# Kernel tuning notes

Hardware: AMD Instinct MI355X
Metric: run time of the kernel (lower is better)

Reference implementation:

```python
import jax, jax.numpy as jnp
import numpy as np

B, H, L, C = 16, 512, 4096, 1
LAM = 0.001  # kernel squash threshold (lam in LongConvKernel)


def setup_inputs() -> dict:
    key = jax.random.key(0)
    ks = jax.random.split(key, 5)
    u = jax.random.normal(ks[0], (B, H, L), jnp.float32)
    # LongConvKernel 'double_exp' init: K ~ N(0, 0.02^2) * exp(-(j/L) * (H//2)^(i/H))
    K = jax.random.normal(ks[1], (C, H, L), jnp.float32) * 0.02
    i = jnp.arange(H, dtype=jnp.float32)[:, None]
    j = jnp.arange(L, dtype=jnp.float32)[None, :]
    double_exp = jnp.exp(-(j / L) * jnp.power(float(H // 2), i / H))  # (H, L)
    kernel = K * double_exp[None]
    D = jax.random.normal(ks[2], (C, H), jnp.float32)  # skip connection params
    # TransposedLinear(C*H -> H): weight (d_output, d_input), kaiming-ish scale
    Wout = jax.random.normal(ks[3], (H, C * H), jnp.float32) / np.sqrt(C * H)
    bout = jax.random.normal(ks[4], (H,), jnp.float32) * 0.01
    return {"u": u, "kernel": kernel, "D": D, "Wout": Wout, "bout": bout}


def reference(u, kernel, D, Wout, bout):
    Lseq = u.shape[-1]
    # kernel squashing: relu(|k| - lam) * sign(k)  (soft-threshold)
    k = jax.nn.relu(jnp.abs(kernel) - LAM) * jnp.sign(kernel)  # (C, H, L)
    n = 2 * Lseq
    k_f = jnp.fft.rfft(k, n=n, axis=-1)            # (C, H, n//2+1) complex
    u_f = jnp.fft.rfft(u, n=n, axis=-1)            # (B, H, n//2+1) complex
    y_f = jnp.einsum('bhl,chl->bchl', u_f, k_f)    # pointwise multiply in freq
    y = jnp.fft.irfft(y_f, n=n, axis=-1)[..., :Lseq]  # (B, C, H, L)
    y = y + jnp.einsum('bhl,ch->bchl', u, D)       # skip term
    y = y.reshape(y.shape[0], C * H, Lseq)         # (B, C*H, L)
    y = jax.nn.gelu(y, approximate=False)          # activation (torch GELU = exact)
    # output_linear: TransposedLinear + swish postact
    y = jnp.einsum('bul,vu->bvl', y, Wout) + bout[None, :, None]
    y = jax.nn.silu(y)
    return y
```

## Files before the change

kernel.cpp:

```cpp
#include <hip/hip_runtime.h>
#include <hip/hip_bf16.h>
#include <math.h>

#define BB 16
#define HH 512
#define LL 4096
#define NFFT 8192
#define LAM 0.001f

typedef __attribute__((ext_vector_type(8))) short short8;
typedef __attribute__((ext_vector_type(4))) float floatx4;

__device__ __forceinline__ void cmul(float ar, float ai, float br, float bi,
                                     float& cr, float& ci) {
  cr = ar * br - ai * bi;
  ci = ar * bi + ai * br;
}

constexpr float W16C[10] = {1.f, 0.92387953f, 0.70710678f, 0.38268343f, 0.f,
                            -0.38268343f, -0.70710678f, -0.92387953f, -1.f, -0.92387953f};
constexpr float W16S[10] = {0.f, -0.38268343f, -0.70710678f, -0.92387953f, -1.f,
                            -0.92387953f, -0.70710678f, -0.38268343f, 0.f, 0.38268343f};
constexpr float W32C[16] = {1.f, 0.98078528f, 0.92387953f, 0.83146961f, 0.70710678f,
                            0.55557023f, 0.38268343f, 0.19509032f, 0.f, -0.19509032f,
                            -0.38268343f, -0.55557023f, -0.70710678f, -0.83146961f,
                            -0.92387953f, -0.98078528f};
constexpr float W32S[16] = {0.f, -0.19509032f, -0.38268343f, -0.55557023f, -0.70710678f,
                            -0.83146961f, -0.92387953f, -0.98078528f, -1.f, -0.98078528f,
                            -0.92387953f, -0.83146961f, -0.70710678f, -0.55557023f,
                            -0.38268343f, -0.19509032f};

__device__ __forceinline__ void fft16_f(float* xr, float* xi) {
  float yr[16], yi[16];
#pragma unroll
  for (int j = 0; j < 4; ++j) {
    float t0r = xr[j] + xr[j + 8],      t0i = xi[j] + xi[j + 8];
    float t1r = xr[j] - xr[j + 8],      t1i = xi[j] - xi[j + 8];
    float t2r = xr[j + 4] + xr[j + 12], t2i = xi[j + 4] + xi[j + 12];
    float t3r = xr[j + 4] - xr[j + 12], t3i = xi[j + 4] - xi[j + 12];
    float o0r = t0r + t2r, o0i = t0i + t2i;
    float o1r = t1r + t3i, o1i = t1i - t3r;
    float o2r = t0r - t2r, o2i = t0i - t2i;
    float o3r = t1r - t3i, o3i = t1i + t3r;
    yr[j] = o0r; yi[j] = o0i;
    if (j == 0) {
      yr[4] = o1r; yi[4] = o1i; yr[8] = o2r; yi[8] = o2i; yr[12] = o3r; yi[12] = o3i;
    } else {
      cmul(o1r, o1i, W16C[j], W16S[j], yr[j + 4], yi[j + 4]);
      cmul(o2r, o2i, W16C[2 * j], W16S[2 * j], yr[j + 8], yi[j + 8]);
      cmul(o3r, o3i, W16C[3 * j], W16S[3 * j], yr[j + 12], yi[j + 12]);
    }
  }
#pragma unroll
  for (int m = 0; m < 4; ++m) {
    float t0r = yr[4 * m] + yr[4 * m + 2],     t0i = yi[4 * m] + yi[4 * m + 2];
    float t1r = yr[4 * m] - yr[4 * m + 2],     t1i = yi[4 * m] - yi[4 * m + 2];
    float t2r = yr[4 * m + 1] + yr[4 * m + 3], t2i = yi[4 * m + 1] + yi[4 * m + 3];
    float t3r = yr[4 * m + 1] - yr[4 * m + 3], t3i = yi[4 * m + 1] - yi[4 * m + 3];
    xr[m] = t0r + t2r;       xi[m] = t0i + t2i;
    xr[m + 4] = t1r + t3i;   xi[m + 4] = t1i - t3r;
    xr[m + 8] = t0r - t2r;   xi[m + 8] = t0i - t2i;
    xr[m + 12] = t1r - t3i;  xi[m + 12] = t1i + t3r;
  }
}

__device__ __forceinline__ void ifft16_f(float* xr, float* xi) {
  float yr[16], yi[16];
#pragma unroll
  for (int m = 0; m < 4; ++m) {
    float t0r = xr[m] + xr[m + 8],      t0i = xi[m] + xi[m + 8];
    float t1r = xr[m] - xr[m + 8],      t1i = xi[m] - xi[m + 8];
    float t2r = xr[m + 4] + xr[m + 12], t2i = xi[m + 4] + xi[m + 12];
    float t3r = xr[m + 4] - xr[m + 12], t3i = xi[m + 4] - xi[m + 12];
    yr[4 * m] = t0r + t2r;     yi[4 * m] = t0i + t2i;
    yr[4 * m + 1] = t1r - t3i; yi[4 * m + 1] = t1i + t3r;
    yr[4 * m + 2] = t0r - t2r; yi[4 * m + 2] = t0i - t2i;
    yr[4 * m + 3] = t1r + t3i; yi[4 * m + 3] = t1i - t3r;
  }
#pragma unroll
  for (int j = 0; j < 4; ++j) {
    float v0r = yr[j], v0i = yi[j];
    float v1r, v1i, v2r, v2i, v3r, v3i;
    if (j == 0) {
      v1r = yr[4]; v1i = yi[4]; v2r = yr[8]; v2i = yi[8]; v3r = yr[12]; v3i = yi[12];
    } else {
      cmul(yr[j + 4], yi[j + 4], W16C[j], -W16S[j], v1r, v1i);
      cmul(yr[j + 8], yi[j + 8], W16C[2 * j], -W16S[2 * j], v2r, v2i);
      cmul(yr[j + 12], yi[j + 12], W16C[3 * j], -W16S[3 * j], v3r, v3i);
    }
    float t0r = v0r + v2r, t0i = v0i + v2i;
    float t1r = v0r - v2r, t1i = v0i - v2i;
    float t2r = v1r + v3r, t2i = v1i + v3i;
    float t3r = v1r - v3r, t3i = v1i - v3i;
    xr[j] = t0r + t2r;       xi[j] = t0i + t2i;
    xr[j + 4] = t1r - t3i;   xi[j + 4] = t1i + t3r;
    xr[j + 8] = t0r - t2r;   xi[j + 8] = t0i - t2i;
    xr[j + 12] = t1r + t3i;  xi[j + 12] = t1i - t3r;
  }
}

__device__ __forceinline__ float gelu_exact(float y) {
  return 0.5f * y * (1.f + erff(y * 0.70710678118654752f));
}

__global__ __launch_bounds__(512) void twgen_kernel(float4* __restrict__ tw1,
                                                    float4* __restrict__ tw2) {
  const int j = threadIdx.x;
  const int m2 = blockIdx.x;
  float s0, c0, s1, c1;
  const float a1 = -6.283185307179586f / 8192.f;
  sincosf(a1 * (float)(j * (2 * m2)), &s0, &c0);
  sincosf(a1 * (float)(j * (2 * m2 + 1)), &s1, &c1);
  tw1[m2 * 512 + j] = make_float4(c0, s0, c1, s1);
  if (j < 32) {
    const float a2 = -6.283185307179586f / 512.f;
    sincosf(a2 * (float)(j * (2 * m2)), &s0, &c0);
    sincosf(a2 * (float)(j * (2 * m2 + 1)), &s1, &c1);
    tw2[m2 * 32 + j] = make_float4(c0, s0, c1, s1);
  }
}

__global__ void wconv_kernel(const float* __restrict__ W,
                             __hip_bfloat16* __restrict__ Wb) {
  int i = blockIdx.x * 256 + threadIdx.x;
  Wb[i] = __float2bfloat16(W[i]);
}

__global__ __launch_bounds__(512)
void kf_kernel(const float* __restrict__ kern, const float* __restrict__ D,
               float* __restrict__ Kf, const float4* __restrict__ tw1,
               const float4* __restrict__ tw2) {
  __shared__ __align__(16) float sre[NFFT];
  __shared__ __align__(16) float sim[NFFT];
  const int t = threadIdx.x;
  const int h = blockIdx.x;
  const float* kr = kern + (size_t)h * LL;

  {
    const int j = t;
    float xr[16], xi[16];
#pragma unroll
    for (int r = 0; r < 8; ++r) {
      float kv = kr[j + 512 * r];
      float a = fabsf(kv) - LAM;
      float sq = (a > 0.f) ? ((kv > 0.f) ? a : -a) : 0.f;
      xr[r] = sq * (1.0f / (float)NFFT);
      xi[r] = 0.f;
    }
#pragma unroll
    for (int r = 8; r < 16; ++r) { xr[r] = 0.f; xi[r] = 0.f; }
    fft16_f(xr, xi);
    const int jx = j ^ (((j >> 5) & 7) << 2);
#pragma unroll
    for (int m2 = 0; m2 < 8; ++m2) {
      float4 w = tw1[m2 * 512 + j];
      float tr, ti;
      cmul(xr[2 * m2], xi[2 * m2], w.x, w.y, tr, ti);
      sre[jx + 512 * (2 * m2)] = tr; sim[jx + 512 * (2 * m2)] = ti;
      cmul(xr[2 * m2 + 1], xi[2 * m2 + 1], w.z, w.w, tr, ti);
      sre[jx + 512 * (2 * m2 + 1)] = tr; sim[jx + 512 * (2 * m2 + 1)] = ti;
    }
  }
  __syncthreads();

  {
    const int jj = t & 31, gg = t >> 5;
    const int base = gg * 512 + jj;
    float xr[16], xi[16];
#pragma unroll
    for (int m = 0; m < 16; ++m) {
      const int a = (base + 32 * m) ^ ((m & 7) << 2);
      xr[m] = sre[a]; xi[m] = sim[a];
    }
    fft16_f(xr, xi);
#pragma unroll
    for (int m2 = 0; m2 < 8; ++m2) {
      float4 w = tw2[m2 * 32 + jj];
      float tr, ti;
      int a0 = (base + 32 * (2 * m2)) ^ (((2 * m2) & 7) << 2);
      cmul(xr[2 * m2], xi[2 * m2], w.x, w.y, tr, ti);
      sre[a0] = tr; sim[a0] = ti;
      int a1 = (base + 32 * (2 * m2 + 1)) ^ (((2 * m2 + 1) & 7) << 2);
      cmul(xr[2 * m2 + 1], xi[2 * m2 + 1], w.z, w.w, tr, ti);
      sre[a1] = tr; sim[a1] = ti;
    }
  }
  __syncthreads();

  {
    const int k = t >> 1, par = t & 1;
    const int kx = k & 7;
    const float sgn = par ? -1.f : 1.f;
    float xr[16], xi[16];
#pragma unroll
    for (int c = 0; c < 4; ++c) {
      float4 lr = ((const float4*)sre)[8 * k + (c ^ kx)];
      float4 hr = ((const float4*)sre)[8 * k + ((c + 4) ^ kx)];
      float4 li = ((const float4*)sim)[8 * k + (c ^ kx)];
      float4 hi4 = ((const float4*)sim)[8 * k + ((c + 4) ^ kx)];
      float vr[4] = {lr.x + sgn * hr.x, lr.y + sgn * hr.y, lr.z + sgn * hr.z, lr.w + sgn * hr.w};
      float vi[4] = {li.x + sgn * hi4.x, li.y + sgn * hi4.y, li.z + sgn * hi4.z, li.w + sgn * hi4.w};
#pragma unroll
      for (int e = 0; e < 4; ++e) {
        const int j = 4 * c + e;
        const float twr = par ? W32C[j] : 1.f;
        const float tws = par ? W32S[j] : 0.f;
        cmul(vr[e], vi[e], twr, tws, xr[j], xi[j]);
      }
    }
    fft16_f(xr, xi);
    const float dsc = D[h] * (1.0f / (float)NFFT);
    float4* out4 = (float4*)(Kf + (size_t)h * NFFT * 2) + 8 * t;
#pragma unroll
    for (int c = 0; c < 8; ++c)
      out4[c] = make_float4(xr[2 * c] + dsc, xi[2 * c], xr[2 * c + 1] + dsc, xi[2 * c + 1]);
  }
}

__global__ __launch_bounds__(512)
void fftconv_kernel(
    const float* __restrict__ u, const float* __restrict__ Kf,
    __hip_bfloat16* __restrict__ g, const float4* __restrict__ tw1,
    const float4* __restrict__ tw2) {
  __shared__ __align__(16) float sre[NFFT];
  __shared__ __align__(16) float sim[NFFT];
  const int t = threadIdx.x;
  const int h = blockIdx.x;
  const int p = blockIdx.y;
  const int b0 = 2 * p, b1 = 2 * p + 1;
  const float* u0 = u + ((size_t)(b0 * HH + h)) * LL;
  const float* u1 = u + ((size_t)(b1 * HH + h)) * LL;

  const int jx = t ^ (((t >> 5) & 7) << 2);

  {
    const int j = t;
    float xr[16], xi[16];
#pragma unroll
    for (int r = 0; r < 8; ++r) {
      xr[r] = u0[j + 512 * r];
      xi[r] = u1[j + 512 * r];
    }
#pragma unroll
    for (int r = 8; r < 16; ++r) { xr[r] = 0.f; xi[r] = 0.f; }
    fft16_f(xr, xi);
#pragma unroll
    for (int m2 = 0; m2 < 8; ++m2) {
      float4 w = tw1[m2 * 512 + j];
      float tr, ti;
      cmul(xr[2 * m2], xi[2 * m2], w.x, w.y, tr, ti);
      sre[jx + 512 * (2 * m2)] = tr; sim[jx + 512 * (2 * m2)] = ti;
      cmul(xr[2 * m2 + 1], xi[2 * m2 + 1], w.z, w.w, tr, ti);
      sre[jx + 512 * (2 * m2 + 1)] = tr; sim[jx + 512 * (2 * m2 + 1)] = ti;
    }
  }
  __syncthreads();

  {
    const int jj = t & 31, gg = t >> 5;
    const int base = gg * 512 + jj;
    float xr[16], xi[16];
#pragma unroll
    for (int m = 0; m < 16; ++m) {
      const int a = (base + 32 * m) ^ ((m & 7) << 2);
      xr[m] = sre[a]; xi[m] = sim[a];
    }
    fft16_f(xr, xi);
#pragma unroll
    for (int m2 = 0; m2 < 8; ++m2) {
      float4 w = tw2[m2 * 32 + jj];
      float tr, ti;
      int a0 = (base + 32 * (2 * m2)) ^ (((2 * m2) & 7) << 2);
      cmul(xr[2 * m2], xi[2 * m2], w.x, w.y, tr, ti);
      sre[a0] = tr; sim[a0] = ti;
      int a1 = (base + 32 * (2 * m2 + 1)) ^ (((2 * m2 + 1) & 7) << 2);
      cmul(xr[2 * m2 + 1], xi[2 * m2 + 1], w.z, w.w, tr, ti);
      sre[a1] = tr; sim[a1] = ti;
    }
  }
  __syncthreads();

  {
    const int k = t >> 1, par = t & 1;
    const int kx = k & 7;
    const float sgn = par ? -1.f : 1.f;
    float xr[16], xi[16];
#pragma unroll
    for (int c = 0; c < 4; ++c) {
      float4 lr = ((const float4*)sre)[8 * k + (c ^ kx)];
      float4 hr = ((const float4*)sre)[8 * k + ((c + 4) ^ kx)];
      float4 li = ((const float4*)sim)[8 * k + (c ^ kx)];
      float4 hi4 = ((const float4*)sim)[8 * k + ((c + 4) ^ kx)];
      float vr[4] = {lr.x + sgn * hr.x, lr.y + sgn * hr.y, lr.z + sgn * hr.z, lr.w + sgn * hr.w};
      float vi[4] = {li.x + sgn * hi4.x, li.y + sgn * hi4.y, li.z + sgn * hi4.z, li.w + sgn * hi4.w};
#pragma unroll
      for (int e = 0; e < 4; ++e) {
        const int j = 4 * c + e;
        const float twr = par ? W32C[j] : 1.f;
        const float tws = par ? W32S[j] : 0.f;
        cmul(vr[e], vi[e], twr, tws, xr[j], xi[j]);
      }
    }
    fft16_f(xr, xi);
    const float4* kf4 = (const float4*)(Kf + (size_t)h * NFFT * 2) + 8 * t;
#pragma unroll
    for (int c = 0; c < 8; ++c) {
      float4 kk = kf4[c];
      float tr, ti;
      cmul(xr[2 * c], xi[2 * c], kk.x, kk.y, tr, ti);
      xr[2 * c] = tr; xi[2 * c] = ti;
      cmul(xr[2 * c + 1], xi[2 * c + 1], kk.z, kk.w, tr, ti);
      xr[2 * c + 1] = tr; xi[2 * c + 1] = ti;
    }
    ifft16_f(xr, xi);
    float outr[16], outi[16];
#pragma unroll
    for (int j = 0; j < 16; ++j) {
      float pr, pi;
      if (par) cmul(xr[j], xi[j], W32C[j], -W32S[j], pr, pi);
      else { pr = xr[j]; pi = xi[j]; }
      float qr = __shfl_xor(pr, 1);
      float qi = __shfl_xor(pi, 1);
      outr[j] = par ? (qr - pr) : (pr + qr);
      outi[j] = par ? (qi - pi) : (pi + qi);
    }
#pragma unroll
    for (int c = 0; c < 4; ++c) {
      const int q = (4 * par + c) ^ kx;
      ((float4*)sre)[8 * k + q] = make_float4(outr[4 * c], outr[4 * c + 1], outr[4 * c + 2], outr[4 * c + 3]);
      ((float4*)sim)[8 * k + q] = make_float4(outi[4 * c], outi[4 * c + 1], outi[4 * c + 2], outi[4 * c + 3]);
    }
  }
  __syncthreads();

  {
    const int jj = t & 31, gg = t >> 5;
    const int base = gg * 512 + jj;
    float yr[16], yi[16];
#pragma unroll
    for (int m2 = 0; m2 < 8; ++m2) {
      float4 w = tw2[m2 * 32 + jj];
      int a0 = (base + 32 * (2 * m2)) ^ (((2 * m2) & 7) << 2);
      cmul(sre[a0], sim[a0], w.x, -w.y, yr[2 * m2], yi[2 * m2]);
      int a1 = (base + 32 * (2 * m2 + 1)) ^ (((2 * m2 + 1) & 7) << 2);
      cmul(sre[a1], sim[a1], w.z, -w.w, yr[2 * m2 + 1], yi[2 * m2 + 1]);
    }
    ifft16_f(yr, yi);
#pragma unroll
    for (int m = 0; m < 16; ++m) {
      const int a = (base + 32 * m) ^ ((m & 7) << 2);
      sre[a] = yr[m]; sim[a] = yi[m];
    }
  }
  __syncthreads();

  {
    const int j = t;
    float yr[16], yi[16];
#pragma unroll
    for (int m2 = 0; m2 < 8; ++m2) {
      float4 w = tw1[m2 * 512 + j];
      cmul(sre[jx + 512 * (2 * m2)], sim[jx + 512 * (2 * m2)], w.x, -w.y,
           yr[2 * m2], yi[2 * m2]);
      cmul(sre[jx + 512 * (2 * m2 + 1)], sim[jx + 512 * (2 * m2 + 1)], w.z, -w.w,
           yr[2 * m2 + 1], yi[2 * m2 + 1]);
    }
    ifft16_f(yr, yi);
    __hip_bfloat16* g0 = g + ((size_t)(b0 * HH + h)) * LL;
    __hip_bfloat16* g1 = g + ((size_t)(b1 * HH + h)) * LL;
#pragma unroll
    for (int r = 0; r < 8; ++r) {
      g0[j + 512 * r] = __float2bfloat16(gelu_exact(yr[r]));
      g1[j + 512 * r] = __float2bfloat16(gelu_exact(yi[r]));
    }
  }
}

__global__ __launch_bounds__(256) void transpose_kernel(
    const __hip_bfloat16* __restrict__ g, __hip_bfloat16* __restrict__ g2) {
  __shared__ unsigned short tile[64][72];
  const int lb = blockIdx.x;
  const int hb = blockIdx.y;
  const int b = blockIdx.z;
  const int l0 = lb * 64, h0 = hb * 64;
  const int tid = threadIdx.x;
  const int r = tid >> 3;
  const int gc = tid & 7;
  const int c = gc * 8;
  const unsigned short* gs = (const unsigned short*)g;
  unsigned short* g2s = (unsigned short*)g2;
  for (int it = 0; it < 2; ++it) {
    int rr = r + it * 32;
    int4 v = *(const int4*)(gs + ((size_t)(b * HH + h0 + rr)) * LL + l0 + c);
    *(int4*)&tile[rr][(gc ^ (rr >> 3)) << 3] = v;
  }
  __syncthreads();
  for (int it = 0; it < 2; ++it) {
    int rr = r + it * 32;
    const int pc = (rr & 7) | (((rr >> 3) ^ gc) << 3);
    unsigned short vals[8];
#pragma unroll
    for (int j = 0; j < 8; ++j) vals[j] = tile[c + j][pc];
    *(int4*)(g2s + ((size_t)(b * LL + l0 + rr)) * HH + h0 + c) = *(int4*)vals;
  }
}

__global__ __launch_bounds__(256, 4) void gemm_kernel(
    const __hip_bfloat16* __restrict__ Wb, const __hip_bfloat16* __restrict__ g2,
    const float* __restrict__ bout, float* __restrict__ out) {
  const int vt = blockIdx.x;
  const int lt = blockIdx.y;
  const int b = blockIdx.z;
  const int wave = threadIdx.x >> 6;
  const int ln = threadIdx.x & 63;
  const int wr = wave >> 1, wc = wave & 1;
  const int vbase = vt * 128 + wr * 64;
  const int lbase = lt * 128 + wc * 64;
  const int lane16 = ln & 15;
  const int quad = ln >> 4;

  floatx4 acc[4][4];
#pragma unroll
  for (int mi = 0; mi < 4; ++mi)
#pragma unroll
    for (int ni = 0; ni < 4; ++ni) acc[mi][ni] = (floatx4){0.f, 0.f, 0.f, 0.f};

  const unsigned short* A = (const unsigned short*)Wb;
  const unsigned short* Bm = (const unsigned short*)g2 + (size_t)b * LL * HH;

  for (int k0 = 0; k0 < HH; k0 += 32) {
    const int kk = k0 + quad * 8;
    short8 af[4], bf[4];
#pragma unroll
    for (int mi = 0; mi < 4; ++mi) {
      const int m = vbase + mi * 16 + lane16;
      af[mi] = *(const short8*)(A + (size_t)m * HH + kk);
    }
#pragma unroll
    for (int ni = 0; ni < 4; ++ni) {
      const int n = lbase + ni * 16 + lane16;
      bf[ni] = *(const short8*)(Bm + (size_t)n * HH + kk);
    }
#pragma unroll
    for (int mi = 0; mi < 4; ++mi)
#pragma unroll
      for (int ni = 0; ni < 4; ++ni)
        acc[mi][ni] = __builtin_amdgcn_mfma_f32_16x16x32_bf16(af[mi], bf[ni],
                                                              acc[mi][ni], 0, 0, 0);
  }

#pragma unroll
  for (int mi = 0; mi < 4; ++mi) {
#pragma unroll
    for (int r = 0; r < 4; ++r) {
      const int m = vbase + mi * 16 + quad * 4 + r;
      const float bias = bout[m];
#pragma unroll
      for (int ni = 0; ni < 4; ++ni) {
        const int n = lbase + ni * 16 + lane16;
        float y = acc[mi][ni][r] + bias;
        y = y / (1.f + __expf(-y));
        out[((size_t)(b * HH + m)) * LL + n] = y;
      }
    }
  }
}

extern "C" void kernel_launch(void* const* d_in, const int* in_sizes, int n_in,
                              void* d_out, int out_size, void* d_ws, size_t ws_size,
                              hipStream_t stream) {
  const float* u = (const float*)d_in[0];
  const float* kern = (const float*)d_in[1];
  const float* D = (const float*)d_in[2];
  const float* Wout = (const float*)d_in[3];
  const float* bout = (const float*)d_in[4];
  float* out = (float*)d_out;

  char* ws = (char*)d_ws;
  const size_t KF_BYTES = (size_t)HH * NFFT * sizeof(float2);
  const size_t G_BYTES = (size_t)BB * HH * LL * 2;
  float* Kf = (float*)ws;
  __hip_bfloat16* g = (__hip_bfloat16*)(ws + KF_BYTES);
  __hip_bfloat16* g2 = (__hip_bfloat16*)(ws + KF_BYTES + G_BYTES);
  __hip_bfloat16* Wb = (__hip_bfloat16*)(ws + KF_BYTES + 2 * G_BYTES);
  float4* tw1 = (float4*)g2;
  float4* tw2 = tw1 + 8 * 512;

  twgen_kernel<<<dim3(8), dim3(512), 0, stream>>>(tw1, tw2);
  wconv_kernel<<<dim3((HH * HH) / 256), dim3(256), 0, stream>>>(Wout, Wb);
  kf_kernel<<<dim3(HH), dim3(512), 0, stream>>>(kern, D, Kf, tw1, tw2);
  fftconv_kernel<<<dim3(HH, BB / 2), dim3(512), 0, stream>>>(u, Kf, g, tw1, tw2);
  transpose_kernel<<<dim3(LL / 64, HH / 64, BB), dim3(256), 0, stream>>>(g, g2);
  gemm_kernel<<<dim3(HH / 128, LL / 128, BB), dim3(256), 0, stream>>>(Wb, g2, bout, out);
}
```

Measured before the change: 588.8 us.

## Restructure 8192-point FFT as radix-8 passes with 1024 threads and interleaved smem

Replaces the radix-16/32 three-pass FFT (512 threads, 16 complex values per thread, split re/im shared arrays) with a radix-8 decomposition: 1024 threads each hold 8 values across four passes. Shared memory becomes one interleaved float2 array with an XOR swizzle, and twiddle tables are regenerated in bit-reversed order. The goal is lower register pressure and more threads per block, better latency hiding and fewer bank conflicts. In exchange it adds extra synchronised passes through shared memory and more block-level barriers.

```diff
diff --git a/kernel.cpp b/kernel.cpp
--- a/kernel.cpp
+++ b/kernel.cpp
@@ -11,112 +11,200 @@
 typedef __attribute__((ext_vector_type(8))) short short8;
 typedef __attribute__((ext_vector_type(4))) float floatx4;
 
+#define R2C 0.70710678118654752f
+
 __device__ __forceinline__ void cmul(float ar, float ai, float br, float bi,
                                      float& cr, float& ci) {
   cr = ar * br - ai * bi;
   ci = ar * bi + ai * br;
 }
 
-constexpr float W16C[10] = {1.f, 0.92387953f, 0.70710678f, 0.38268343f, 0.f,
-                            -0.38268343f, -0.70710678f, -0.92387953f, -1.f, -0.92387953f};
-constexpr float W16S[10] = {0.f, -0.38268343f, -0.70710678f, -0.92387953f, -1.f,
-                            -0.92387953f, -0.70710678f, -0.38268343f, 0.f, 0.38268343f};
-constexpr float W32C[16] = {1.f, 0.98078528f, 0.92387953f, 0.83146961f, 0.70710678f,
-                            0.55557023f, 0.38268343f, 0.19509032f, 0.f, -0.19509032f,
-                            -0.38268343f, -0.55557023f, -0.70710678f, -0.83146961f,
-                            -0.92387953f, -0.98078528f};
-constexpr float W32S[16] = {0.f, -0.19509032f, -0.38268343f, -0.55557023f, -0.70710678f,
-                            -0.83146961f, -0.92387953f, -0.98078528f, -1.f, -0.98078528f,
-                            -0.92387953f, -0.83146961f, -0.70710678f, -0.55557023f,
-                            -0.38268343f, -0.19509032f};
-
-__device__ __forceinline__ void fft16_f(float* xr, float* xi) {
-  float yr[16], yi[16];
-#pragma unroll
-  for (int j = 0; j < 4; ++j) {
-    float t0r = xr[j] + xr[j + 8],      t0i = xi[j] + xi[j + 8];
-    float t1r = xr[j] - xr[j + 8],      t1i = xi[j] - xi[j + 8];
-    float t2r = xr[j + 4] + xr[j + 12], t2i = xi[j + 4] + xi[j + 12];
-    float t3r = xr[j + 4] - xr[j + 12], t3i = xi[j + 4] - xi[j + 12];
-    float o0r = t0r + t2r, o0i = t0i + t2i;
-    float o1r = t1r + t3i, o1i = t1i - t3r;
-    float o2r = t0r - t2r, o2i = t0i - t2i;
-    float o3r = t1r - t3i, o3i = t1i + t3r;
-    yr[j] = o0r; yi[j] = o0i;
-    if (j == 0) {
-      yr[4] = o1r; yi[4] = o1i; yr[8] = o2r; yi[8] = o2i; yr[12] = o3r; yi[12] = o3i;
-    } else {
-      cmul(o1r, o1i, W16C[j], W16S[j], yr[j + 4], yi[j + 4]);
-      cmul(o2r, o2i, W16C[2 * j], W16S[2 * j], yr[j + 8], yi[j + 8]);
-      cmul(o3r, o3i, W16C[3 * j], W16S[3 * j], yr[j + 12], yi[j + 12]);
-    }
-  }
-#pragma unroll
-  for (int m = 0; m < 4; ++m) {
-    float t0r = yr[4 * m] + yr[4 * m + 2],     t0i = yi[4 * m] + yi[4 * m + 2];
-    float t1r = yr[4 * m] - yr[4 * m + 2],     t1i = yi[4 * m] - yi[4 * m + 2];
-    float t2r = yr[4 * m + 1] + yr[4 * m + 3], t2i = yi[4 * m + 1] + yi[4 * m + 3];
-    float t3r = yr[4 * m + 1] - yr[4 * m + 3], t3i = yi[4 * m + 1] - yi[4 * m + 3];
-    xr[m] = t0r + t2r;       xi[m] = t0i + t2i;
-    xr[m + 4] = t1r + t3i;   xi[m + 4] = t1i - t3r;
-    xr[m + 8] = t0r - t2r;   xi[m + 8] = t0i - t2i;
-    xr[m + 12] = t1r - t3i;  xi[m + 12] = t1i + t3r;
-  }
-}
-
-__device__ __forceinline__ void ifft16_f(float* xr, float* xi) {
-  float yr[16], yi[16];
-#pragma unroll
-  for (int m = 0; m < 4; ++m) {
-    float t0r = xr[m] + xr[m + 8],      t0i = xi[m] + xi[m + 8];
-    float t1r = xr[m] - xr[m + 8],      t1i = xi[m] - xi[m + 8];
-    float t2r = xr[m + 4] + xr[m + 12], t2i = xi[m + 4] + xi[m + 12];
-    float t3r = xr[m + 4] - xr[m + 12], t3i = xi[m + 4] - xi[m + 12];
-    yr[4 * m] = t0r + t2r;     yi[4 * m] = t0i + t2i;
-    yr[4 * m + 1] = t1r - t3i; yi[4 * m + 1] = t1i + t3r;
-    yr[4 * m + 2] = t0r - t2r; yi[4 * m + 2] = t0i - t2i;
-    yr[4 * m + 3] = t1r + t3i; yi[4 * m + 3] = t1i - t3r;
-  }
-#pragma unroll
-  for (int j = 0; j < 4; ++j) {
-    float v0r = yr[j], v0i = yi[j];
-    float v1r, v1i, v2r, v2i, v3r, v3i;
-    if (j == 0) {
-      v1r = yr[4]; v1i = yi[4]; v2r = yr[8]; v2i = yi[8]; v3r = yr[12]; v3i = yi[12];
-    } else {
-      cmul(yr[j + 4], yi[j + 4], W16C[j], -W16S[j], v1r, v1i);
-      cmul(yr[j + 8], yi[j + 8], W16C[2 * j], -W16S[2 * j], v2r, v2i);
-      cmul(yr[j + 12], yi[j + 12], W16C[3 * j], -W16S[3 * j], v3r, v3i);
-    }
-    float t0r = v0r + v2r, t0i = v0i + v2i;
-    float t1r = v0r - v2r, t1i = v0i - v2i;
-    float t2r = v1r + v3r, t2i = v1i + v3i;
-    float t3r = v1r - v3r, t3i = v1i - v3i;
-    xr[j] = t0r + t2r;       xi[j] = t0i + t2i;
-    xr[j + 4] = t1r - t3i;   xi[j + 4] = t1i + t3r;
-    xr[j + 8] = t0r - t2r;   xi[j + 8] = t0i - t2i;
-    xr[j + 12] = t1r + t3i;  xi[j + 12] = t1i - t3r;
-  }
+constexpr float W16C[8] = {1.f, 0.92387953f, 0.70710678f, 0.38268343f, 0.f,
+                           -0.38268343f, -0.70710678f, -0.92387953f};
+constexpr float W16S[8] = {0.f, -0.38268343f, -0.70710678f, -0.92387953f, -1.f,
+                           -0.92387953f, -0.70710678f, -0.38268343f};
+constexpr int BR8[8] = {0, 4, 2, 6, 1, 5, 3, 7};
+constexpr float W16CB[8] = {W16C[0], W16C[4], W16C[2], W16C[6],
+                            W16C[1], W16C[5], W16C[3], W16C[7]};
+constexpr float W16SB[8] = {W16S[0], W16S[4], W16S[2], W16S[6],
+                            W16S[1], W16S[5], W16S[3], W16S[7]};
+
+__device__ __forceinline__ int slotf(int a) { return a ^ ((a >> 4) & 15); }
+
+__device__ __forceinline__ void fft8(float* r, float* i) {
+  float t0r = r[0] + r[4], t0i = i[0] + i[4], u0r = r[0] - r[4], u0i = i[0] - i[4];
+  float t1r = r[1] + r[5], t1i = i[1] + i[5], u1r = r[1] - r[5], u1i = i[1] - i[5];
+  float t2r = r[2] + r[6], t2i = i[2] + i[6], u2r = r[2] - r[6], u2i = i[2] - i[6];
+  float t3r = r[3] + r[7], t3i = i[3] + i[7], u3r = r[3] - r[7], u3i = i[3] - i[7];
+  float w1r = R2C * (u1r + u1i), w1i = R2C * (u1i - u1r);
+  float w2r = u2i, w2i = -u2r;
+  float w3r = R2C * (u3i - u3r), w3i = -R2C * (u3r + u3i);
+  float p0r = t0r + t2r, p0i = t0i + t2i, q0r = t0r - t2r, q0i = t0i - t2i;
+  float p1r = t1r + t3r, p1i = t1i + t3i, q1r = t1r - t3r, q1i = t1i - t3i;
+  float s1r = q1i, s1i = -q1r;
+  float v0r = u0r + w2r, v0i = u0i + w2i, x0r = u0r - w2r, x0i = u0i - w2i;
+  float v1r = w1r + w3r, v1i = w1i + w3i, x1r = w1r - w3r, x1i = w1i - w3i;
+  float y1r = x1i, y1i = -x1r;
+  r[0] = p0r + p1r; i[0] = p0i + p1i;
+  r[1] = p0r - p1r; i[1] = p0i - p1i;
+  r[2] = q0r + s1r; i[2] = q0i + s1i;
+  r[3] = q0r - s1r; i[3] = q0i - s1i;
+  r[4] = v0r + v1r; i[4] = v0i + v1i;
+  r[5] = v0r - v1r; i[5] = v0i - v1i;
+  r[6] = x0r + y1r; i[6] = x0i + y1i;
+  r[7] = x0r - y1r; i[7] = x0i - y1i;
+}
+
+__device__ __forceinline__ void ifft8(float* r, float* i) {
+  float p0r = r[0] + r[1], p0i = i[0] + i[1];
+  float p1r = r[0] - r[1], p1i = i[0] - i[1];
+  float q0r = r[2] + r[3], q0i = i[2] + i[3];
+  float s1r = r[2] - r[3], s1i = i[2] - i[3];
+  float v0r = r[4] + r[5], v0i = i[4] + i[5];
+  float v1r = r[4] - r[5], v1i = i[4] - i[5];
+  float x0r = r[6] + r[7], x0i = i[6] + i[7];
+  float y1r = r[6] - r[7], y1i = i[6] - i[7];
+  float q1r = -s1i, q1i = s1r;
+  float x1r = -y1i, x1i = y1r;
+  float t0r = p0r + q0r, t0i = p0i + q0i, t2r = p0r - q0r, t2i = p0i - q0i;
+  float t1r = p1r + q1r, t1i = p1i + q1i, t3r = p1r - q1r, t3i = p1i - q1i;
+  float a0r = v0r + x0r, a0i = v0i + x0i, a2r = v0r - x0r, a2i = v0i - x0i;
+  float a1r = v1r + x1r, a1i = v1i + x1i, a3r = v1r - x1r, a3i = v1i - x1i;
+  float u1r = R2C * (a1r - a1i), u1i = R2C * (a1r + a1i);
+  float u2r = -a2i, u2i = a2r;
+  float u3r = -R2C * (a3r + a3i), u3i = R2C * (a3r - a3i);
+  r[0] = t0r + a0r; i[0] = t0i + a0i;  r[4] = t0r - a0r; i[4] = t0i - a0i;
+  r[1] = t1r + u1r; i[1] = t1i + u1i;  r[5] = t1r - u1r; i[5] = t1i - u1i;
+  r[2] = t2r + u2r; i[2] = t2i + u2i;  r[6] = t2r - u2r; i[6] = t2i - u2i;
+  r[3] = t3r + u3r; i[3] = t3i + u3i;  r[7] = t3r - u3r; i[7] = t3i - u3i;
 }
 
 __device__ __forceinline__ float gelu_exact(float y) {
   return 0.5f * y * (1.f + erff(y * 0.70710678118654752f));
 }
 
-__global__ __launch_bounds__(512) void twgen_kernel(float4* __restrict__ tw1,
-                                                    float4* __restrict__ tw2) {
+template <int LOGJ>
+__device__ __forceinline__ void r8_fwd(float2* sb, int t, const float4* tw) {
+  const int J = 1 << LOGJ;
+  const int j = t & (J - 1);
+  const int base = (t >> LOGJ) << (LOGJ + 3);
+  float xr[8], xi[8];
+#pragma unroll
+  for (int s = 0; s < 8; ++s) {
+    float2 v = sb[slotf(base + j + (s << LOGJ))];
+    xr[s] = v.x; xi[s] = v.y;
+  }
+  fft8(xr, xi);
+#pragma unroll
+  for (int q = 0; q < 4; ++q) {
+    float4 w = tw[(q << LOGJ) + j];
+    float tr, ti;
+    cmul(xr[2 * q], xi[2 * q], w.x, w.y, tr, ti);
+    sb[slotf(base + (BR8[2 * q] << LOGJ) + j)] = make_float2(tr, ti);
+    cmul(xr[2 * q + 1], xi[2 * q + 1], w.z, w.w, tr, ti);
+    sb[slotf(base + (BR8[2 * q + 1] << LOGJ) + j)] = make_float2(tr, ti);
+  }
+}
+
+template <int LOGJ>
+__device__ __forceinline__ void r8_inv(float2* sb, int t, const float4* tw) {
+  const int J = 1 << LOGJ;
+  const int j = t & (J - 1);
+  const int base = (t >> LOGJ) << (LOGJ + 3);
+  float xr[8], xi[8];
+#pragma unroll
+  for (int q = 0; q < 4; ++q) {
+    float4 w = tw[(q << LOGJ) + j];
+    float2 v0 = sb[slotf(base + (BR8[2 * q] << LOGJ) + j)];
+    cmul(v0.x, v0.y, w.x, -w.y, xr[2 * q], xi[2 * q]);
+    float2 v1 = sb[slotf(base + (BR8[2 * q + 1] << LOGJ) + j)];
+    cmul(v1.x, v1.y, w.z, -w.w, xr[2 * q + 1], xi[2 * q + 1]);
+  }
+  ifft8(xr, xi);
+#pragma unroll
+  for (int s = 0; s < 8; ++s)
+    sb[slotf(base + j + (s << LOGJ))] = make_float2(xr[s], xi[s]);
+}
+
+__device__ __forceinline__ void p1_scatter(float2* sb, int j, const float4* tw1,
+                                           float* xr, float* xi) {
+  fft8(xr, xi);
+#pragma unroll
+  for (int q = 0; q < 4; ++q) {
+    float4 w = tw1[(q << 10) + j];
+    float tr, ti;
+    cmul(xr[2 * q], xi[2 * q], w.x, w.y, tr, ti);
+    sb[slotf((BR8[2 * q] << 10) + j)] = make_float2(tr, ti);
+    cmul(xr[2 * q + 1], xi[2 * q + 1], w.z, w.w, tr, ti);
+    sb[slotf((BR8[2 * q + 1] << 10) + j)] = make_float2(tr, ti);
+  }
+}
+
+__device__ __forceinline__ void p4_bins(float2* sb, int t, float* br_, float* bi_) {
+  const int p = t >> 1, par = t & 1;
+  const int a0 = (p << 4) + par;
+  float xr[8], xi[8];
+#pragma unroll
+  for (int e = 0; e < 8; ++e) {
+    float2 v = sb[slotf(a0 + 2 * e)];
+    xr[e] = v.x; xi[e] = v.y;
+  }
+  fft8(xr, xi);
+#pragma unroll
+  for (int s = 0; s < 8; ++s) {
+    float tr, ti;
+    if (par) { cmul(xr[s], xi[s], W16CB[s], W16SB[s], tr, ti); }
+    else { tr = xr[s]; ti = xi[s]; }
+    float orr = __shfl_xor(tr, 1);
+    float oii = __shfl_xor(ti, 1);
+    br_[s] = par ? (orr - tr) : (tr + orr);
+    bi_[s] = par ? (oii - ti) : (ti + oii);
+  }
+}
+
+__device__ __forceinline__ void p4_inv(float2* sb, int t, float* br_, float* bi_) {
+  const int p = t >> 1, par = t & 1;
+  const int a0 = (p << 4) + par;
+  float yr[8], yi[8];
+#pragma unroll
+  for (int s = 0; s < 8; ++s) {
+    float orr = __shfl_xor(br_[s], 1);
+    float oii = __shfl_xor(bi_[s], 1);
+    float er = par ? (orr - br_[s]) : (br_[s] + orr);
+    float ei = par ? (oii - bi_[s]) : (bi_[s] + oii);
+    if (par) { float tr, ti; cmul(er, ei, W16CB[s], -W16SB[s], tr, ti); er = tr; ei = ti; }
+    yr[s] = er; yi[s] = ei;
+  }
+  ifft8(yr, yi);
+#pragma unroll
+  for (int e = 0; e < 8; ++e)
+    sb[slotf(a0 + 2 * e)] = make_float2(yr[e], yi[e]);
+}
+
+__global__ __launch_bounds__(1024) void twgen_kernel(float4* __restrict__ tw1,
+                                                     float4* __restrict__ tw2,
+                                                     float4* __restrict__ tw3) {
   const int j = threadIdx.x;
-  const int m2 = blockIdx.x;
-  float s0, c0, s1, c1;
-  const float a1 = -6.283185307179586f / 8192.f;
-  sincosf(a1 * (float)(j * (2 * m2)), &s0, &c0);
-  sincosf(a1 * (float)(j * (2 * m2 + 1)), &s1, &c1);
-  tw1[m2 * 512 + j] = make_float4(c0, s0, c1, s1);
-  if (j < 32) {
-    const float a2 = -6.283185307179586f / 512.f;
-    sincosf(a2 * (float)(j * (2 * m2)), &s0, &c0);
-    sincosf(a2 * (float)(j * (2 * m2 + 1)), &s1, &c1);
-    tw2[m2 * 32 + j] = make_float4(c0, s0, c1, s1);
+#pragma unroll
+  for (int q = 0; q < 4; ++q) {
+    const int m0 = BR8[2 * q], m1 = BR8[2 * q + 1];
+    float s0, c0, s1, c1;
+    const float a1 = -6.283185307179586f / 8192.f;
+    sincosf(a1 * (float)(j * m0), &s0, &c0);
+    sincosf(a1 * (float)(j * m1), &s1, &c1);
+    tw1[(q << 10) + j] = make_float4(c0, s0, c1, s1);
+    if (j < 128) {
+      const float a2 = -6.283185307179586f / 1024.f;
+      sincosf(a2 * (float)(j * m0), &s0, &c0);
+      sincosf(a2 * (float)(j * m1), &s1, &c1);
+      tw2[(q << 7) + j] = make_float4(c0, s0, c1, s1);
+    }
+    if (j < 16) {
+      const float a3 = -6.283185307179586f / 128.f;
+      sincosf(a3 * (float)(j * m0), &s0, &c0);
+      sincosf(a3 * (float)(j * m1), &s1, &c1);
+      tw3[(q << 4) + j] = make_float4(c0, s0, c1, s1);
+    }
   }
 }
 
@@ -126,104 +214,50 @@
   Wb[i] = __float2bfloat16(W[i]);
 }
 
-__global__ __launch_bounds__(512)
+__global__ __launch_bounds__(1024)
 void kf_kernel(const float* __restrict__ kern, const float* __restrict__ D,
                float* __restrict__ Kf, const float4* __restrict__ tw1,
-               const float4* __restrict__ tw2) {
-  __shared__ __align__(16) float sre[NFFT];
-  __shared__ __align__(16) float sim[NFFT];
+               const float4* __restrict__ tw2, const float4* __restrict__ tw3) {
+  __shared__ __align__(16) float2 sb[NFFT];
   const int t = threadIdx.x;
   const int h = blockIdx.x;
   const float* kr = kern + (size_t)h * LL;
-
   {
-    const int j = t;
-    float xr[16], xi[16];
-#pragma unroll
-    for (int r = 0; r < 8; ++r) {
-      float kv = kr[j + 512 * r];
+    float xr[8], xi[8];
+#pragma unroll
+    for (int s = 0; s < 4; ++s) {
+      float kv = kr[t + (s << 10)];
       float a = fabsf(kv) - LAM;
       float sq = (a > 0.f) ? ((kv > 0.f) ? a : -a) : 0.f;
-      xr[r] = sq * (1.0f / (float)NFFT);
-      xi[r] = 0.f;
-    }
-#pragma unroll
-    for (int r = 8; r < 16; ++r) { xr[r] = 0.f; xi[r] = 0.f; }
-    fft16_f(xr, xi);
-    const int jx = j ^ (((j >> 5) & 7) << 2);
-#pragma unroll
-    for (int m2 = 0; m2 < 8; ++m2) {
-      float4 w = tw1[m2 * 512 + j];
-      float tr, ti;
-      cmul(xr[2 * m2], xi[2 * m2], w.x, w.y, tr, ti);
-      sre[jx + 512 * (2 * m2)] = tr; sim[jx + 512 * (2 * m2)] = ti;
-      cmul(xr[2 * m2 + 1], xi[2 * m2 + 1], w.z, w.w, tr, ti);
-      sre[jx + 512 * (2 * m2 + 1)] = tr; sim[jx + 512 * (2 * m2 + 1)] = ti;
-    }
-  }
-  __syncthreads();
-
+      xr[s] = sq * (1.f / 8192.f);
+      xi[s] = 0.f;
+    }
+#pragma unroll
+    for (int s = 4; s < 8; ++s) { xr[s] = 0.f; xi[s] = 0.f; }
+    p1_scatter(sb, t, tw1, xr, xi);
+  }
+  __syncthreads();
+  r8_fwd<7>(sb, t, tw2);
+  __syncthreads();
+  r8_fwd<4>(sb, t, tw3);
+  __syncthreads();
   {
-    const int jj = t & 31, gg = t >> 5;
-    const int base = gg * 512 + jj;
-    float xr[16], xi[16];
-#pragma unroll
-    for (int m = 0; m < 16; ++m) {
-      const int a = (base + 32 * m) ^ ((m & 7) << 2);
-      xr[m] = sre[a]; xi[m] = sim[a];
-    }
-    fft16_f(xr, xi);
-#pragma unroll
-    for (int m2 = 0; m2 < 8; ++m2) {
-      float4 w = tw2[m2 * 32 + jj];
-      float tr, ti;
-      int a0 = (base + 32 * (2 * m2)) ^ (((2 * m2) & 7) << 2);
-      cmul(xr[2 * m2], xi[2 * m2], w.x, w.y, tr, ti);
-      sre[a0] = tr; sim[a0] = ti;
-      int a1 = (base + 32 * (2 * m2 + 1)) ^ (((2 * m2 + 1) & 7) << 2);
-      cmul(xr[2 * m2 + 1], xi[2 * m2 + 1], w.z, w.w, tr, ti);
-      sre[a1] = tr; sim[a1] = ti;
-    }
-  }
-  __syncthreads();
-
-  {
-    const int k = t >> 1, par = t & 1;
-    const int kx = k & 7;
-    const float sgn = par ? -1.f : 1.f;
-    float xr[16], xi[16];
-#pragma unroll
-    for (int c = 0; c < 4; ++c) {
-      float4 lr = ((const float4*)sre)[8 * k + (c ^ kx)];
-      float4 hr = ((const float4*)sre)[8 * k + ((c + 4) ^ kx)];
-      float4 li = ((const float4*)sim)[8 * k + (c ^ kx)];
-      float4 hi4 = ((const float4*)sim)[8 * k + ((c + 4) ^ kx)];
-      float vr[4] = {lr.x + sgn * hr.x, lr.y + sgn * hr.y, lr.z + sgn * hr.z, lr.w + sgn * hr.w};
-      float vi[4] = {li.x + sgn * hi4.x, li.y + sgn * hi4.y, li.z + sgn * hi4.z, li.w + sgn * hi4.w};
-#pragma unroll
-      for (int e = 0; e < 4; ++e) {
-        const int j = 4 * c + e;
-        const float twr = par ? W32C[j] : 1.f;
-        const float tws = par ? W32S[j] : 0.f;
-        cmul(vr[e], vi[e], twr, tws, xr[j], xi[j]);
-      }
-    }
-    fft16_f(xr, xi);
-    const float dsc = D[h] * (1.0f / (float)NFFT);
-    float4* out4 = (float4*)(Kf + (size_t)h * NFFT * 2) + 8 * t;
-#pragma unroll
-    for (int c = 0; c < 8; ++c)
-      out4[c] = make_float4(xr[2 * c] + dsc, xi[2 * c], xr[2 * c + 1] + dsc, xi[2 * c + 1]);
-  }
-}
-
-__global__ __launch_bounds__(512)
-void fftconv_kernel(
-    const float* __restrict__ u, const float* __restrict__ Kf,
-    __hip_bfloat16* __restrict__ g, const float4* __restrict__ tw1,
-    const float4* __restrict__ tw2) {
-  __shared__ __align__(16) float sre[NFFT];
-  __shared__ __align__(16) float sim[NFFT];
+    float br_[8], bi_[8];
+    p4_bins(sb, t, br_, bi_);
+    const float dsc = D[h] * (1.f / 8192.f);
+    float4* out4 = (float4*)(Kf + (size_t)h * NFFT * 2) + (t << 2);
+#pragma unroll
+    for (int q = 0; q < 4; ++q)
+      out4[q] = make_float4(br_[2 * q] + dsc, bi_[2 * q],
+                            br_[2 * q + 1] + dsc, bi_[2 * q + 1]);
+  }
+}
+
+__global__ __launch_bounds__(1024)
+void fftconv_kernel(const float* __restrict__ u, const float* __restrict__ Kf,
+                    __hip_bfloat16* __restrict__ g, const float4* __restrict__ tw1,
+                    const float4* __restrict__ tw2, const float4* __restrict__ tw3) {
+  __shared__ __align__(16) float2 sb[NFFT];
   const int t = threadIdx.x;
   const int h = blockIdx.x;
   const int p = blockIdx.y;
@@ -231,147 +265,59 @@
   const float* u0 = u + ((size_t)(b0 * HH + h)) * LL;
   const float* u1 = u + ((size_t)(b1 * HH + h)) * LL;
 
-  const int jx = t ^ (((t >> 5) & 7) << 2);
-
   {
-    const int j = t;
-    float xr[16], xi[16];
-#pragma unroll
-    for (int r = 0; r < 8; ++r) {
-      xr[r] = u0[j + 512 * r];
-      xi[r] = u1[j + 512 * r];
-    }
-#pragma unroll
-    for (int r = 8; r < 16; ++r) { xr[r] = 0.f; xi[r] = 0.f; }
-    fft16_f(xr, xi);
-#pragma unroll
-    for (int m2 = 0; m2 < 8; ++m2) {
-      float4 w = tw1[m2 * 512 + j];
+    float xr[8], xi[8];
+#pragma unroll
+    for (int s = 0; s < 4; ++s) {
+      xr[s] = u0[t + (s << 10)];
+      xi[s] = u1[t + (s << 10)];
+    }
+#pragma unroll
+    for (int s = 4; s < 8; ++s) { xr[s] = 0.f; xi[s] = 0.f; }
+    p1_scatter(sb, t, tw1, xr, xi);
+  }
+  __syncthreads();
+  r8_fwd<7>(sb, t, tw2);
+  __syncthreads();
+  r8_fwd<4>(sb, t, tw3);
+  __syncthreads();
+  {
+    float br_[8], bi_[8];
+    p4_bins(sb, t, br_, bi_);
+    const float4* kf4 = (const float4*)(Kf + (size_t)h * NFFT * 2) + (t << 2);
+#pragma unroll
+    for (int q = 0; q < 4; ++q) {
+      float4 kk = kf4[q];
       float tr, ti;
-      cmul(xr[2 * m2], xi[2 * m2], w.x, w.y, tr, ti);
-      sre[jx + 512 * (2 * m2)] = tr; sim[jx + 512 * (2 * m2)] = ti;
-      cmul(xr[2 * m2 + 1], xi[2 * m2 + 1], w.z, w.w, tr, ti);
-      sre[jx + 512 * (2 * m2 + 1)] = tr; sim[jx + 512 * (2 * m2 + 1)] = ti;
-    }
-  }
-  __syncthreads();
-
+      cmul(br_[2 * q], bi_[2 * q], kk.x, kk.y, tr, ti);
+      br_[2 * q] = tr; bi_[2 * q] = ti;
+      cmul(br_[2 * q + 1], bi_[2 * q + 1], kk.z, kk.w, tr, ti);
+      br_[2 * q + 1] = tr; bi_[2 * q + 1] = ti;
+    }
+    p4_inv(sb, t, br_, bi_);
+  }
+  __syncthreads();
+  r8_inv<4>(sb, t, tw3);
+  __syncthreads();
+  r8_inv<7>(sb, t, tw2);
+  __syncthreads();
   {
-    const int jj = t & 31, gg = t >> 5;
-    const int base = gg * 512 + jj;
-    float xr[16], xi[16];
-#pragma unroll
-    for (int m = 0; m < 16; ++m) {
-      const int a = (base + 32 * m) ^ ((m & 7) << 2);
-      xr[m] = sre[a]; xi[m] = sim[a];
-    }
-    fft16_f(xr, xi);
-#pragma unroll
-    for (int m2 = 0; m2 < 8; ++m2) {
-      float4 w = tw2[m2 * 32 + jj];
-      float tr, ti;
-      int a0 = (base + 32 * (2 * m2)) ^ (((2 * m2) & 7) << 2);
-      cmul(xr[2 * m2], xi[2 * m2], w.x, w.y, tr, ti);
-      sre[a0] = tr; sim[a0] = ti;
-      int a1 = (base + 32 * (2 * m2 + 1)) ^ (((2 * m2 + 1) & 7) << 2);
-      cmul(xr[2 * m2 + 1], xi[2 * m2 + 1], w.z, w.w, tr, ti);
-      sre[a1] = tr; sim[a1] = ti;
-    }
-  }
-  __syncthreads();
-
-  {
-    const int k = t >> 1, par = t & 1;
-    const int kx = k & 7;
-    const float sgn = par ? -1.f : 1.f;
-    float xr[16], xi[16];
-#pragma unroll
-    for (int c = 0; c < 4; ++c) {
-      float4 lr = ((const float4*)sre)[8 * k + (c ^ kx)];
-      float4 hr = ((const float4*)sre)[8 * k + ((c + 4) ^ kx)];
-      float4 li = ((const float4*)sim)[8 * k + (c ^ kx)];
-      float4 hi4 = ((const float4*)sim)[8 * k + ((c + 4) ^ kx)];
-      float vr[4] = {lr.x + sgn * hr.x, lr.y + sgn * hr.y, lr.z + sgn * hr.z, lr.w + sgn * hr.w};
-      float vi[4] = {li.x + sgn * hi4.x, li.y + sgn * hi4.y, li.z + sgn * hi4.z, li.w + sgn * hi4.w};
-#pragma unroll
-      for (int e = 0; e < 4; ++e) {
-        const int j = 4 * c + e;
-        const float twr = par ? W32C[j] : 1.f;
-        const float tws = par ? W32S[j] : 0.f;
-        cmul(vr[e], vi[e], twr, tws, xr[j], xi[j]);
-      }
-    }
-    fft16_f(xr, xi);
-    const float4* kf4 = (const float4*)(Kf + (size_t)h * NFFT * 2) + 8 * t;
-#pragma unroll
-    for (int c = 0; c < 8; ++c) {
-      float4 kk = kf4[c];
-      float tr, ti;
-      cmul(xr[2 * c], xi[2 * c], kk.x, kk.y, tr, ti);
-      xr[2 * c] = tr; xi[2 * c] = ti;
-      cmul(xr[2 * c + 1], xi[2 * c + 1], kk.z, kk.w, tr, ti);
-      xr[2 * c + 1] = tr; xi[2 * c + 1] = ti;
-    }
-    ifft16_f(xr, xi);
-    float outr[16], outi[16];
-#pragma unroll
-    for (int j = 0; j < 16; ++j) {
-      float pr, pi;
-      if (par) cmul(xr[j], xi[j], W32C[j], -W32S[j], pr, pi);
-      else { pr = xr[j]; pi = xi[j]; }
-      float qr = __shfl_xor(pr, 1);
-      float qi = __shfl_xor(pi, 1);
-      outr[j] = par ? (qr - pr) : (pr + qr);
-      outi[j] = par ? (qi - pi) : (pi + qi);
-    }
-#pragma unroll
-    for (int c = 0; c < 4; ++c) {
-      const int q = (4 * par + c) ^ kx;
-      ((float4*)sre)[8 * k + q] = make_float4(outr[4 * c], outr[4 * c + 1], outr[4 * c + 2], outr[4 * c + 3]);
-      ((float4*)sim)[8 * k + q] = make_float4(outi[4 * c], outi[4 * c + 1], outi[4 * c + 2], outi[4 * c + 3]);
-    }
-  }
-  __syncthreads();
-
-  {
-    const int jj = t & 31, gg = t >> 5;
-    const int base = gg * 512 + jj;
-    float yr[16], yi[16];
-#pragma unroll
-    for (int m2 = 0; m2 < 8; ++m2) {
-      float4 w = tw2[m2 * 32 + jj];
-      int a0 = (base + 32 * (2 * m2)) ^ (((2 * m2) & 7) << 2);
-      cmul(sre[a0], sim[a0], w.x, -w.y, yr[2 * m2], yi[2 * m2]);
-      int a1 = (base + 32 * (2 * m2 + 1)) ^ (((2 * m2 + 1) & 7) << 2);
-      cmul(sre[a1], sim[a1], w.z, -w.w, yr[2 * m2 + 1], yi[2 * m2 + 1]);
-    }
-    ifft16_f(yr, yi);
-#pragma unroll
-    for (int m = 0; m < 16; ++m) {
-      const int a = (base + 32 * m) ^ ((m & 7) << 2);
-      sre[a] = yr[m]; sim[a] = yi[m];
-    }
-  }
-  __syncthreads();
-
-  {
-    const int j = t;
-    float yr[16], yi[16];
-#pragma unroll
-    for (int m2 = 0; m2 < 8; ++m2) {
-      float4 w = tw1[m2 * 512 + j];
-      cmul(sre[jx + 512 * (2 * m2)], sim[jx + 512 * (2 * m2)], w.x, -w.y,
-           yr[2 * m2], yi[2 * m2]);
-      cmul(sre[jx + 512 * (2 * m2 + 1)], sim[jx + 512 * (2 * m2 + 1)], w.z, -w.w,
-           yr[2 * m2 + 1], yi[2 * m2 + 1]);
-    }
-    ifft16_f(yr, yi);
+    float xr[8], xi[8];
+#pragma unroll
+    for (int q = 0; q < 4; ++q) {
+      float4 w = tw1[(q << 10) + t];
+      float2 v0 = sb[slotf((BR8[2 * q] << 10) + t)];
+      cmul(v0.x, v0.y, w.x, -w.y, xr[2 * q], xi[2 * q]);
+      float2 v1 = sb[slotf((BR8[2 * q + 1] << 10) + t)];
+      cmul(v1.x, v1.y, w.z, -w.w, xr[2 * q + 1], xi[2 * q + 1]);
+    }
+    ifft8(xr, xi);
     __hip_bfloat16* g0 = g + ((size_t)(b0 * HH + h)) * LL;
     __hip_bfloat16* g1 = g + ((size_t)(b1 * HH + h)) * LL;
 #pragma unroll
-    for (int r = 0; r < 8; ++r) {
-      g0[j + 512 * r] = __float2bfloat16(gelu_exact(yr[r]));
-      g1[j + 512 * r] = __float2bfloat16(gelu_exact(yi[r]));
+    for (int s = 0; s < 4; ++s) {
+      g0[t + (s << 10)] = __float2bfloat16(gelu_exact(xr[s]));
+      g1[t + (s << 10)] = __float2bfloat16(gelu_exact(xi[s]));
     }
   }
 }
@@ -484,12 +430,13 @@
   __hip_bfloat16* g2 = (__hip_bfloat16*)(ws + KF_BYTES + G_BYTES);
   __hip_bfloat16* Wb = (__hip_bfloat16*)(ws + KF_BYTES + 2 * G_BYTES);
   float4* tw1 = (float4*)g2;
-  float4* tw2 = tw1 + 8 * 512;
-
-  twgen_kernel<<<dim3(8), dim3(512), 0, stream>>>(tw1, tw2);
+  float4* tw2 = tw1 + 4 * 1024;
+  float4* tw3 = tw2 + 4 * 128;
+
+  twgen_kernel<<<dim3(1), dim3(1024), 0, stream>>>(tw1, tw2, tw3);
   wconv_kernel<<<dim3((HH * HH) / 256), dim3(256), 0, stream>>>(Wout, Wb);
-  kf_kernel<<<dim3(HH), dim3(512), 0, stream>>>(kern, D, Kf, tw1, tw2);
-  fftconv_kernel<<<dim3(HH, BB / 2), dim3(512), 0, stream>>>(u, Kf, g, tw1, tw2);
+  kf_kernel<<<dim3(HH), dim3(1024), 0, stream>>>(kern, D, Kf, tw1, tw2, tw3);
+  fftconv_kernel<<<dim3(HH, BB / 2), dim3(1024), 0, stream>>>(u, Kf, g, tw1, tw2, tw3);
   transpose_kernel<<<dim3(LL / 64, HH / 64, BB), dim3(256), 0, stream>>>(g, g2);
   gemm_kernel<<<dim3(HH / 128, LL / 128, BB), dim3(256), 0, stream>>>(Wb, g2, bout, out);
 }
```

New measurement: 554.8 us. 5.8% less time.
